# Performance work log

Hardware: AMD Instinct MI355X
Metric: run time of the kernel (lower is better)

## Reference

```python
import jax, jax.numpy as jnp
import numpy as np

N, D, K = 200000, 512, 256


def setup_inputs() -> dict:
    key = jax.random.key(0)
    ks = jax.random.split(key, 7)
    scale_in = 1.0 / np.sqrt(D)
    scale_k = 1.0 / np.sqrt(K)
    return {
        "embeds": jax.random.normal(ks[0], (N, D), dtype=jnp.float32),
        "W1": jax.random.normal(ks[1], (K, D), dtype=jnp.float32) * scale_in,
        "b1": jnp.zeros((K,), dtype=jnp.float32),
        "W2": jax.random.normal(ks[2], (K, K), dtype=jnp.float32) * scale_k,
        "b2": jnp.zeros((K,), dtype=jnp.float32),
        "W3": jax.random.normal(ks[3], (K, K), dtype=jnp.float32) * scale_k,
        "b3": jnp.zeros((K,), dtype=jnp.float32),
    }


def reference(embeds, W1, b1, W2, b2, W3, b3):
    # estimation MLP: Linear -> LeakyReLU -> Linear -> LeakyReLU -> Linear
    x = jax.nn.leaky_relu(embeds @ W1.T + b1, negative_slope=0.01)   # [N, K]
    x = jax.nn.leaky_relu(x @ W2.T + b2, negative_slope=0.01)        # [N, K]
    x = x @ W3.T + b3                                                # [N, K]
    gamma = jax.nn.softmax(x, axis=-1)                               # [N, K]
    cluster_indices = jnp.argmax(gamma, axis=-1)                     # [N]

    gamma_sum = jnp.sum(gamma, axis=0)                               # [K]
    target_gamma = jax.nn.softmax(gamma ** 2 / gamma_sum, axis=-1)   # [N, K]

    # mean: algebraically gamma^T @ embeds (avoids O(N*K*D) intermediate)
    mean = jnp.einsum('nk,nd->kd', gamma, embeds) / gamma_sum[:, None]  # [K, D]

    # F.kl_div(target_gamma.log(), gamma, reduction='sum')
    # = sum(gamma * (log gamma - log target_gamma))
    kl_loss = jnp.sum(gamma * (jnp.log(gamma) - jnp.log(target_gamma)))
    return (kl_loss, cluster_indices, mean)
```

## Files before the change

### kernel.cpp

```cpp
#include <hip/hip_runtime.h>
#include <math.h>

#define NROWS 200000
#define DIM   512
#define KC    256
#define BM    64
#define NBLK_MLP (NROWS / BM)
#define NSTEPS   (NROWS / 32)
#define MCHUNKS  125
#define MSTEPS   (NSTEPS / MCHUNKS)
#define MARGIN   0.0625f

typedef float f32x4 __attribute__((ext_vector_type(4)));
typedef short short8v __attribute__((ext_vector_type(8)));
typedef short short4v __attribute__((ext_vector_type(4)));

__device__ inline short f2bs(float f) {
  unsigned u = __float_as_uint(f);
  unsigned r = (u + 0x7FFFu + ((u >> 16) & 1u)) >> 16;
  return (short)r;
}
__device__ inline float bs2f(short s) {
  return __uint_as_float(((unsigned)(unsigned short)s) << 16);
}

__global__ __launch_bounds__(256) void transpose_kernel(const float* __restrict__ src,
                                                        float* __restrict__ dst,
                                                        int R, int C) {
  __shared__ float tile[32][33];
  const int tx = threadIdx.x;
  const int ty = threadIdx.y;
  const int c0 = blockIdx.x * 32;
  const int r0 = blockIdx.y * 32;
#pragma unroll
  for (int j = 0; j < 32; j += 8)
    tile[ty + j][tx] = src[(size_t)(r0 + ty + j) * C + c0 + tx];
  __syncthreads();
#pragma unroll
  for (int j = 0; j < 32; j += 8)
    dst[(size_t)(c0 + ty + j) * R + r0 + tx] = tile[tx][ty + j];
}

__global__ __launch_bounds__(256) void packW_kernel(const float* __restrict__ W,
                                                    short* __restrict__ P, int Kin) {
  const int KS = Kin >> 5;
  const int total = 16 * KS * 64;
  int tid = blockIdx.x * 256 + threadIdx.x;
  if (tid >= total) return;
  const int l = tid & 63;
  const int ks = (tid >> 6) % KS;
  const int nf = tid / (64 * KS);
  const float* src = W + (size_t)(nf * 16 + (l & 15)) * Kin + ks * 32 + (l >> 4) * 8;
  short8v v;
#pragma unroll
  for (int j = 0; j < 8; ++j) v[j] = f2bs(src[j]);
  *(short8v*)(P + (size_t)tid * 8) = v;
}

__global__ __launch_bounds__(256) void packE_kernel(const float* __restrict__ E,
                                                    short* __restrict__ EP) {
  const size_t s = (size_t)blockIdx.x * 256 + threadIdx.x;
  const int lane = (int)(s & 63);
  const int df = (int)((s >> 6) & 31);
  const int ns = (int)(s >> 11);
  if (ns >= NSTEPS) return;
  const int lo = lane & 15, q = lane >> 4;
  const float* src = E + ((size_t)ns * 32 + q * 8) * DIM + df * 16 + lo;
  short8v v;
#pragma unroll
  for (int j = 0; j < 8; ++j) v[j] = f2bs(src[(size_t)j * DIM]);
  *(short8v*)(EP + s * 8) = v;
}

__global__ __launch_bounds__(256, 4) void mlp_mfma_kernel(
    const float* __restrict__ E,
    const short* __restrict__ PW1, const short* __restrict__ PW2,
    const short* __restrict__ PW3,
    const float* __restrict__ b1, const float* __restrict__ b2,
    const float* __restrict__ b3,
    short* __restrict__ gammaP, float* __restrict__ idx_out,
    float* __restrict__ gsp, int* __restrict__ tiecnt, int* __restrict__ tielist) {
  __shared__ __align__(16) short X[BM * 256];
  __shared__ float redV[4][BM];
  __shared__ float redI[4][BM];
  __shared__ float red2[4][BM];
  __shared__ float rowM[BM];
  __shared__ float rowS[BM];
  __shared__ int lrows[BM];
  __shared__ int lcnt;
  __shared__ int gbase;

  const int t = threadIdx.x;
  const int blk = blockIdx.x;
  const int wc = t >> 6;
  const int lane = t & 63;
  const int lo = lane & 15;
  const int q = lane >> 4;

  if (t == 0) lcnt = 0;

  f32x4 acc[4][4];

#pragma unroll
  for (int m = 0; m < 4; ++m)
#pragma unroll
    for (int n = 0; n < 4; ++n) acc[m][n] = (f32x4){0.f, 0.f, 0.f, 0.f};

  const float* e0 = E + (size_t)(blk * BM + lo) * DIM + q * 8;
#pragma unroll
  for (int ks = 0; ks < 16; ++ks) {
    short8v a[4];
#pragma unroll
    for (int m = 0; m < 4; ++m) {
      const float* ep = e0 + m * 16 * DIM + ks * 32;
      float4 x0 = *(const float4*)ep;
      float4 x1 = *(const float4*)(ep + 4);
      short8v av;
      av[0] = f2bs(x0.x); av[1] = f2bs(x0.y); av[2] = f2bs(x0.z); av[3] = f2bs(x0.w);
      av[4] = f2bs(x1.x); av[5] = f2bs(x1.y); av[6] = f2bs(x1.z); av[7] = f2bs(x1.w);
      a[m] = av;
    }
#pragma unroll
    for (int n = 0; n < 4; ++n) {
      short8v b = *(const short8v*)(PW1 + ((size_t)((wc * 4 + n) * 16 + ks) * 64 + lane) * 8);
#pragma unroll
      for (int m = 0; m < 4; ++m)
        acc[m][n] = __builtin_amdgcn_mfma_f32_16x16x32_bf16(a[m], b, acc[m][n], 0, 0, 0);
    }
  }
  {
    float bc[4];
#pragma unroll
    for (int n = 0; n < 4; ++n) bc[n] = b1[wc * 64 + n * 16 + lo];
#pragma unroll
    for (int m = 0; m < 4; ++m)
#pragma unroll
      for (int j = 0; j < 4; ++j) {
        const int row = m * 16 + 4 * q + j;
#pragma unroll
        for (int n = 0; n < 4; ++n) {
          float v = acc[m][n][j] + bc[n];
          v = v > 0.f ? v : 0.01f * v;
          const int col = wc * 64 + n * 16 + lo;
          X[row * 256 + ((((col >> 3) ^ (row & 7)) << 3) | (col & 7))] = f2bs(v);
        }
      }
  }
  __syncthreads();

#pragma unroll
  for (int m = 0; m < 4; ++m)
#pragma unroll
    for (int n = 0; n < 4; ++n) acc[m][n] = (f32x4){0.f, 0.f, 0.f, 0.f};
#pragma unroll
  for (int ks = 0; ks < 8; ++ks) {
    short8v a[4];
#pragma unroll
    for (int m = 0; m < 4; ++m) {
      const int row = m * 16 + lo;
      const int ck = (ks * 4 + q) ^ (row & 7);
      a[m] = *(const short8v*)&X[row * 256 + ck * 8];
    }
#pragma unroll
    for (int n = 0; n < 4; ++n) {
      short8v b = *(const short8v*)(PW2 + ((size_t)((wc * 4 + n) * 8 + ks) * 64 + lane) * 8);
#pragma unroll
      for (int m = 0; m < 4; ++m)
        acc[m][n] = __builtin_amdgcn_mfma_f32_16x16x32_bf16(a[m], b, acc[m][n], 0, 0, 0);
    }
  }
  __syncthreads();
  {
    float bc[4];
#pragma unroll
    for (int n = 0; n < 4; ++n) bc[n] = b2[wc * 64 + n * 16 + lo];
#pragma unroll
    for (int m = 0; m < 4; ++m)
#pragma unroll
      for (int j = 0; j < 4; ++j) {
        const int row = m * 16 + 4 * q + j;
#pragma unroll
        for (int n = 0; n < 4; ++n) {
          float v = acc[m][n][j] + bc[n];
          v = v > 0.f ? v : 0.01f * v;
          const int col = wc * 64 + n * 16 + lo;
          X[row * 256 + ((((col >> 3) ^ (row & 7)) << 3) | (col & 7))] = f2bs(v);
        }
      }
  }
  __syncthreads();

#pragma unroll
  for (int m = 0; m < 4; ++m)
#pragma unroll
    for (int n = 0; n < 4; ++n) acc[m][n] = (f32x4){0.f, 0.f, 0.f, 0.f};
#pragma unroll
  for (int ks = 0; ks < 8; ++ks) {
    short8v a[4];
#pragma unroll
    for (int m = 0; m < 4; ++m) {
      const int row = m * 16 + lo;
      const int ck = (ks * 4 + q) ^ (row & 7);
      a[m] = *(const short8v*)&X[row * 256 + ck * 8];
    }
#pragma unroll
    for (int n = 0; n < 4; ++n) {
      short8v b = *(const short8v*)(PW3 + ((size_t)((wc * 4 + n) * 8 + ks) * 64 + lane) * 8);
#pragma unroll
      for (int m = 0; m < 4; ++m)
        acc[m][n] = __builtin_amdgcn_mfma_f32_16x16x32_bf16(a[m], b, acc[m][n], 0, 0, 0);
    }
  }
  {
    float bc[4];
#pragma unroll
    for (int n = 0; n < 4; ++n) bc[n] = b3[wc * 64 + n * 16 + lo];
#pragma unroll
    for (int m = 0; m < 4; ++m)
#pragma unroll
      for (int n = 0; n < 4; ++n)
#pragma unroll
        for (int j = 0; j < 4; ++j) acc[m][n][j] += bc[n];
  }

#pragma unroll
  for (int m = 0; m < 4; ++m)
#pragma unroll
    for (int j = 0; j < 4; ++j) {
      const int r = m * 16 + 4 * q + j;
      float mx = acc[m][0][j];
      int mi = wc * 64 + lo;
      float m2 = -3.4e38f;
#pragma unroll
      for (int n = 1; n < 4; ++n) {
        float v = acc[m][n][j];
        int c = wc * 64 + n * 16 + lo;
        if (v > mx) { m2 = mx; mx = v; mi = c; }
        else if (v > m2) m2 = v;
      }
#pragma unroll
      for (int off = 1; off < 16; off <<= 1) {
        float ov = __shfl_xor(mx, off, 64);
        int oi = __shfl_xor(mi, off, 64);
        float o2 = __shfl_xor(m2, off, 64);
        float nm2 = fmaxf(m2, o2);
        if (ov > mx) { nm2 = fmaxf(nm2, mx); mx = ov; mi = oi; }
        else { nm2 = fmaxf(nm2, ov); if (ov == mx && oi < mi) mi = oi; }
        m2 = nm2;
      }
      if (lo == 0) { redV[wc][r] = mx; redI[wc][r] = __int_as_float(mi); red2[wc][r] = m2; }
    }
  __syncthreads();

  if (t < BM) {
    float gm = -3.4e38f, g2 = -3.4e38f;
    int gi = 0;
#pragma unroll
    for (int w = 0; w < 4; ++w) {
      float v = redV[w][t];
      int i2 = __float_as_int(redI[w][t]);
      float s2 = red2[w][t];
      if (v > gm) { g2 = fmaxf(fmaxf(g2, gm), s2); gm = v; gi = i2; }
      else { if (v == gm && i2 < gi) gi = i2; g2 = fmaxf(g2, v); }
    }
    rowM[t] = gm;
    idx_out[(size_t)blk * BM + t] = (float)gi;
    if (gm - g2 < MARGIN) { int p = atomicAdd(&lcnt, 1); lrows[p] = blk * BM + t; }
  }
  __syncthreads();

#pragma unroll
  for (int m = 0; m < 4; ++m)
#pragma unroll
    for (int j = 0; j < 4; ++j) {
      const int r = m * 16 + 4 * q + j;
      const float gm = rowM[r];
      float s = 0.f;
#pragma unroll
      for (int n = 0; n < 4; ++n) {
        float e = expf(acc[m][n][j] - gm);
        acc[m][n][j] = e;
        s += e;
      }
#pragma unroll
      for (int off = 1; off < 16; off <<= 1) s += __shfl_xor(s, off, 64);
      if (lo == 0) redV[wc][r] = s;
    }
  __syncthreads();
  if (t < BM) rowS[t] = redV[0][t] + redV[1][t] + redV[2][t] + redV[3][t];
  __syncthreads();

  float csum[4] = {0.f, 0.f, 0.f, 0.f};
#pragma unroll
  for (int m = 0; m < 4; ++m)
#pragma unroll
    for (int j = 0; j < 4; ++j) {
      const int r = m * 16 + 4 * q + j;
      const float inv = 1.0f / rowS[r];
#pragma unroll
      for (int n = 0; n < 4; ++n) {
        float g = acc[m][n][j] * inv;
        csum[n] += g;
        const int col = wc * 64 + n * 16 + lo;
        X[r * 256 + ((((col >> 3) ^ (r & 7)) << 3) | (col & 7))] = f2bs(g);
      }
    }
#pragma unroll
  for (int n = 0; n < 4; ++n) {
    csum[n] += __shfl_xor(csum[n], 16, 64);
    csum[n] += __shfl_xor(csum[n], 32, 64);
  }
  if (q == 0) {
#pragma unroll
    for (int n = 0; n < 4; ++n)
      gsp[(size_t)blk * KC + wc * 64 + n * 16 + lo] = csum[n];
  }
  __syncthreads();

#pragma unroll
  for (int ns = 0; ns < 2; ++ns)
#pragma unroll
    for (int i = 0; i < 4; ++i) {
      const int kf = wc * 4 + i;
      const int k = kf * 16 + lo;
      short8v v;
#pragma unroll
      for (int j = 0; j < 8; ++j) {
        const int r = ns * 32 + q * 8 + j;
        v[j] = X[r * 256 + ((((k >> 3) ^ (r & 7)) << 3) | (k & 7))];
      }
      *(short8v*)(gammaP + ((size_t)((blk * 2 + ns) * 16 + kf) * 64 + lane) * 8) = v;
    }

  if (t == 0 && lcnt > 0) gbase = atomicAdd(tiecnt, lcnt);
  __syncthreads();
  if (t < lcnt) tielist[gbase + t] = lrows[t];
}

__global__ __launch_bounds__(256, 2) void recompute_kernel(
    const float* __restrict__ E,
    const float* __restrict__ W1T, const float* __restrict__ W2T,
    const float* __restrict__ W3T,
    const float* __restrict__ b1, const float* __restrict__ b2,
    const float* __restrict__ b3,
    const int* __restrict__ tiecnt, const int* __restrict__ tielist,
    float* __restrict__ idx_out) {
  __shared__ float Xa[32][KC];
  __shared__ float Xb[32][KC];
  __shared__ float Wt[8][KC];
  __shared__ float Et[8][32];
  __shared__ int rid[32];

  const int t = threadIdx.x;
  const int cg = t & 31;
  const int rg = t >> 5;
  const int cnt = *tiecnt;

  for (int base = blockIdx.x * 32; base < cnt; base += gridDim.x * 32) {
    const int nr = min(32, cnt - base);
    if (t < 32) rid[t] = tielist[base + min(t, nr - 1)];
    __syncthreads();

    float acc[4][2][4];
#pragma unroll
    for (int i = 0; i < 4; ++i)
#pragma unroll
      for (int j = 0; j < 2; ++j)
#pragma unroll
        for (int c = 0; c < 4; ++c) acc[i][j][c] = 0.0f;
    for (int d0 = 0; d0 < DIM; d0 += 8) {
      const float4* wsrc = (const float4*)(W1T + (size_t)d0 * KC);
      float4* wdst = (float4*)(&Wt[0][0]);
      wdst[t] = wsrc[t];
      wdst[t + 256] = wsrc[t + 256];
      Et[t & 7][t >> 3] = E[(size_t)rid[t >> 3] * DIM + d0 + (t & 7)];
      __syncthreads();
#pragma unroll
      for (int dd = 0; dd < 8; ++dd) {
        float4 e4 = *(const float4*)(&Et[dd][rg * 4]);
        float4 w0 = *(const float4*)(&Wt[dd][cg * 4]);
        float4 w1 = *(const float4*)(&Wt[dd][cg * 4 + 128]);
        float ev[4] = {e4.x, e4.y, e4.z, e4.w};
        float wv[2][4] = {{w0.x, w0.y, w0.z, w0.w}, {w1.x, w1.y, w1.z, w1.w}};
#pragma unroll
        for (int i = 0; i < 4; ++i)
#pragma unroll
          for (int j = 0; j < 2; ++j)
#pragma unroll
            for (int c = 0; c < 4; ++c)
              acc[i][j][c] = fmaf(ev[i], wv[j][c], acc[i][j][c]);
      }
      __syncthreads();
    }
    {
      float4 bb0 = *(const float4*)(b1 + cg * 4);
      float4 bb1 = *(const float4*)(b1 + cg * 4 + 128);
      float bv[2][4] = {{bb0.x, bb0.y, bb0.z, bb0.w}, {bb1.x, bb1.y, bb1.z, bb1.w}};
#pragma unroll
      for (int i = 0; i < 4; ++i)
#pragma unroll
        for (int j = 0; j < 2; ++j) {
          float4 v;
          float vv[4];
#pragma unroll
          for (int c = 0; c < 4; ++c) {
            float x = acc[i][j][c] + bv[j][c];
            vv[c] = x > 0.0f ? x : 0.01f * x;
          }
          v.x = vv[0]; v.y = vv[1]; v.z = vv[2]; v.w = vv[3];
          *(float4*)(&Xa[rg * 4 + i][cg * 4 + j * 128]) = v;
        }
    }
    __syncthreads();
#pragma unroll
    for (int i = 0; i < 4; ++i)
#pragma unroll
      for (int j = 0; j < 2; ++j)
#pragma unroll
        for (int c = 0; c < 4; ++c) acc[i][j][c] = 0.0f;
    for (int d0 = 0; d0 < KC; d0 += 8) {
      const float4* wsrc = (const float4*)(W2T + (size_t)d0 * KC);
      float4* wdst = (float4*)(&Wt[0][0]);
      wdst[t] = wsrc[t];
      wdst[t + 256] = wsrc[t + 256];
      __syncthreads();
#pragma unroll
      for (int dd = 0; dd < 8; ++dd) {
        const int d = d0 + dd;
        float ev[4];
#pragma unroll
        for (int i = 0; i < 4; ++i) ev[i] = Xa[rg * 4 + i][d];
        float4 w0 = *(const float4*)(&Wt[dd][cg * 4]);
        float4 w1 = *(const float4*)(&Wt[dd][cg * 4 + 128]);
        float wv[2][4] = {{w0.x, w0.y, w0.z, w0.w}, {w1.x, w1.y, w1.z, w1.w}};
#pragma unroll
        for (int i = 0; i < 4; ++i)
#pragma unroll
          for (int j = 0; j < 2; ++j)
#pragma unroll
            for (int c = 0; c < 4; ++c)
              acc[i][j][c] = fmaf(ev[i], wv[j][c], acc[i][j][c]);
      }
      __syncthreads();
    }
    {
      float4 bb0 = *(const float4*)(b2 + cg * 4);
      float4 bb1 = *(const float4*)(b2 + cg * 4 + 128);
      float bv[2][4] = {{bb0.x, bb0.y, bb0.z, bb0.w}, {bb1.x, bb1.y, bb1.z, bb1.w}};
#pragma unroll
      for (int i = 0; i < 4; ++i)
#pragma unroll
        for (int j = 0; j < 2; ++j) {
          float4 v;
          float vv[4];
#pragma unroll
          for (int c = 0; c < 4; ++c) {
            float x = acc[i][j][c] + bv[j][c];
            vv[c] = x > 0.0f ? x : 0.01f * x;
          }
          v.x = vv[0]; v.y = vv[1]; v.z = vv[2]; v.w = vv[3];
          *(float4*)(&Xb[rg * 4 + i][cg * 4 + j * 128]) = v;
        }
    }
    __syncthreads();
#pragma unroll
    for (int i = 0; i < 4; ++i)
#pragma unroll
      for (int j = 0; j < 2; ++j)
#pragma unroll
        for (int c = 0; c < 4; ++c) acc[i][j][c] = 0.0f;
    for (int d0 = 0; d0 < KC; d0 += 8) {
      const float4* wsrc = (const float4*)(W3T + (size_t)d0 * KC);
      float4* wdst = (float4*)(&Wt[0][0]);
      wdst[t] = wsrc[t];
      wdst[t + 256] = wsrc[t + 256];
      __syncthreads();
#pragma unroll
      for (int dd = 0; dd < 8; ++dd) {
        const int d = d0 + dd;
        float ev[4];
#pragma unroll
        for (int i = 0; i < 4; ++i) ev[i] = Xb[rg * 4 + i][d];
        float4 w0 = *(const float4*)(&Wt[dd][cg * 4]);
        float4 w1 = *(const float4*)(&Wt[dd][cg * 4 + 128]);
        float wv[2][4] = {{w0.x, w0.y, w0.z, w0.w}, {w1.x, w1.y, w1.z, w1.w}};
#pragma unroll
        for (int i = 0; i < 4; ++i)
#pragma unroll
          for (int j = 0; j < 2; ++j)
#pragma unroll
            for (int c = 0; c < 4; ++c)
              acc[i][j][c] = fmaf(ev[i], wv[j][c], acc[i][j][c]);
      }
      __syncthreads();
    }
    {
      float4 bb0 = *(const float4*)(b3 + cg * 4);
      float4 bb1 = *(const float4*)(b3 + cg * 4 + 128);
      float bv[2][4] = {{bb0.x, bb0.y, bb0.z, bb0.w}, {bb1.x, bb1.y, bb1.z, bb1.w}};
#pragma unroll
      for (int i = 0; i < 4; ++i)
#pragma unroll
        for (int j = 0; j < 2; ++j) {
          float4 v;
          v.x = acc[i][j][0] + bv[j][0];
          v.y = acc[i][j][1] + bv[j][1];
          v.z = acc[i][j][2] + bv[j][2];
          v.w = acc[i][j][3] + bv[j][3];
          *(float4*)(&Xa[rg * 4 + i][cg * 4 + j * 128]) = v;
        }
    }
    __syncthreads();
    const int wv_ = t >> 6;
    const int lane = t & 63;
#pragma unroll 1
    for (int rr = 0; rr < 8; ++rr) {
      const int lr = wv_ * 8 + rr;
      float4 x4 = *(const float4*)(&Xa[lr][lane * 4]);
      float xv[4] = {x4.x, x4.y, x4.z, x4.w};
      float bvv = xv[0];
      int bi = lane * 4;
#pragma unroll
      for (int c = 1; c < 4; ++c)
        if (xv[c] > bvv) { bvv = xv[c]; bi = lane * 4 + c; }
#pragma unroll
      for (int off = 32; off > 0; off >>= 1) {
        float ov = __shfl_xor(bvv, off, 64);
        int oi = __shfl_xor(bi, off, 64);
        if (ov > bvv || (ov == bvv && oi < bi)) { bvv = ov; bi = oi; }
      }
      if (lane == 0 && lr < nr) idx_out[rid[lr]] = (float)bi;
    }
    __syncthreads();
  }
}

__global__ __launch_bounds__(256) void gsum_reduce_kernel(const float* __restrict__ gsp,
                                                          float* __restrict__ gsum) {
  const int b = blockIdx.x;
  const int k = threadIdx.x;
  float s = 0.0f;
  for (int i = 0; i < 125; ++i) s += gsp[(size_t)(b * 125 + i) * KC + k];
  atomicAdd(&gsum[k], s);
}

__global__ __launch_bounds__(256) void kl_kernel(const short* __restrict__ gP,
                                                 const float* __restrict__ gsum,
                                                 float* __restrict__ out_kl) {
  const int t = threadIdx.x;
  const int w = t >> 6, lane = t & 63;
  const int lo = lane & 15;
  __shared__ float bsum[4];
  float kacc = 0.f;
#pragma unroll 1
  for (int it = 0; it < 2; ++it) {
    const int ns = blockIdx.x * 8 + w * 2 + it;
    if (ns < NSTEPS) {
      float s12[8], m[8], s[8];
#pragma unroll
      for (int j = 0; j < 8; ++j) { s12[j] = 0.f; m[j] = 0.f; s[j] = 0.f; }
#pragma unroll 1
      for (int kf = 0; kf < 16; ++kf) {
        short8v g8 = *(const short8v*)(gP + ((size_t)(ns * 16 + kf) * 64 + lane) * 8);
        const float rg = 1.0f / gsum[kf * 16 + lo];
#pragma unroll
        for (int j = 0; j < 8; ++j) {
          float g = bs2f(g8[j]);
          float y = g * g * rg;
          s12[j] += (g > 0.f ? g * __logf(g) : 0.f) - g * y;
          float nm = fmaxf(m[j], y);
          s[j] = s[j] * __expf(m[j] - nm) + __expf(y - nm);
          m[j] = nm;
        }
      }
#pragma unroll
      for (int off = 1; off < 16; off <<= 1) {
#pragma unroll
        for (int j = 0; j < 8; ++j) {
          float om = __shfl_xor(m[j], off, 64);
          float os = __shfl_xor(s[j], off, 64);
          float nm = fmaxf(m[j], om);
          s[j] = s[j] * __expf(m[j] - nm) + os * __expf(om - nm);
          m[j] = nm;
          s12[j] += __shfl_xor(s12[j], off, 64);
        }
      }
      if (lo == 0) {
#pragma unroll
        for (int j = 0; j < 8; ++j) kacc += s12[j] + m[j] + __logf(s[j]);
      }
    }
  }
#pragma unroll
  for (int off = 1; off < 64; off <<= 1) kacc += __shfl_xor(kacc, off, 64);
  if (lane == 0) bsum[w] = kacc;
  __syncthreads();
  if (t == 0) atomicAdd(out_kl, bsum[0] + bsum[1] + bsum[2] + bsum[3]);
}

__global__ __launch_bounds__(256, 4) void mean_mfma(const short* __restrict__ gP,
                                                    const short* __restrict__ EP,
                                                    float* __restrict__ partial) {
  const int t = threadIdx.x;
  const int w = t >> 6, lane = t & 63;
  const int kt = blockIdx.x >> 1;
  const int dt = blockIdx.x & 1;
  const int c = blockIdx.y;
  f32x4 acc[4][4];
#pragma unroll
  for (int i = 0; i < 4; ++i)
#pragma unroll
    for (int j = 0; j < 4; ++j) acc[i][j] = (f32x4){0.f, 0.f, 0.f, 0.f};

  const int ns0 = c * MSTEPS;
#pragma unroll 2
  for (int nsi = 0; nsi < MSTEPS; ++nsi) {
    const int ns = ns0 + nsi;
    short8v af[4], bf[4];
#pragma unroll
    for (int i = 0; i < 4; ++i)
      af[i] = *(const short8v*)(gP + ((size_t)(ns * 16 + kt * 4 + i) * 64 + lane) * 8);
#pragma unroll
    for (int j = 0; j < 4; ++j)
      bf[j] = *(const short8v*)(EP + ((size_t)(ns * 32 + dt * 16 + w * 4 + j) * 64 + lane) * 8);
#pragma unroll
    for (int i = 0; i < 4; ++i)
#pragma unroll
      for (int j = 0; j < 4; ++j)
        acc[i][j] = __builtin_amdgcn_mfma_f32_16x16x32_bf16(af[i], bf[j], acc[i][j], 0, 0, 0);
  }
  const int lo = lane & 15, q = lane >> 4;
  const size_t pbase = (size_t)c * (KC * DIM);
#pragma unroll
  for (int i = 0; i < 4; ++i)
#pragma unroll
    for (int j = 0; j < 4; ++j) {
      const int d = dt * 256 + w * 64 + j * 16 + lo;
#pragma unroll
      for (int r = 0; r < 4; ++r) {
        const int k = kt * 64 + i * 16 + q * 4 + r;
        partial[pbase + (size_t)k * DIM + d] = acc[i][j][r];
      }
    }
}

__global__ __launch_bounds__(256) void mean_pass2(const float* __restrict__ partial,
                                                  const float* __restrict__ gsum,
                                                  float* __restrict__ out_mean) {
  const int t = blockIdx.x * 256 + threadIdx.x;
  float s = 0.0f;
  for (int c = 0; c < MCHUNKS; ++c) s += partial[(size_t)c * (KC * DIM) + t];
  out_mean[t] = s / gsum[t >> 9];
}

extern "C" void kernel_launch(void* const* d_in, const int* in_sizes, int n_in,
                              void* d_out, int out_size, void* d_ws, size_t ws_size,
                              hipStream_t stream) {
  const float* E  = (const float*)d_in[0];
  const float* W1 = (const float*)d_in[1];
  const float* b1 = (const float*)d_in[2];
  const float* W2 = (const float*)d_in[3];
  const float* b2 = (const float*)d_in[4];
  const float* W3 = (const float*)d_in[5];
  const float* b3 = (const float*)d_in[6];
  float* out = (float*)d_out;

  char* p = (char*)d_ws;
  short* gammaP = (short*)p; p += (size_t)NROWS * KC * 2;
  short* EPb    = (short*)p; p += (size_t)NROWS * DIM * 2;
  float* gsp    = (float*)p; p += (size_t)NBLK_MLP * KC * 4;
  float* gsum   = (float*)p; p += KC * 4;
  short* pw1    = (short*)p; p += (size_t)KC * DIM * 2;
  short* pw2    = (short*)p; p += (size_t)KC * KC * 2;
  short* pw3    = (short*)p; p += (size_t)KC * KC * 2;
  float* w1t    = (float*)p; p += (size_t)DIM * KC * 4;
  float* w2t    = (float*)p; p += (size_t)KC * KC * 4;
  float* w3t    = (float*)p; p += (size_t)KC * KC * 4;
  int* tcnt     = (int*)p;   p += 256;
  int* tlist    = (int*)p;   p += (size_t)NROWS * 4;
  float* mpart  = (float*)p; p += (size_t)MCHUNKS * KC * DIM * 4;

  hipMemsetAsync(d_out, 0, sizeof(float), stream);
  hipMemsetAsync(gsum, 0, KC * sizeof(float), stream);
  hipMemsetAsync(tcnt, 0, sizeof(int), stream);

  packW_kernel<<<64, 256, 0, stream>>>(W1, pw1, DIM);
  packW_kernel<<<32, 256, 0, stream>>>(W2, pw2, KC);
  packW_kernel<<<32, 256, 0, stream>>>(W3, pw3, KC);
  transpose_kernel<<<dim3(DIM / 32, KC / 32), dim3(32, 8), 0, stream>>>(W1, w1t, KC, DIM);
  transpose_kernel<<<dim3(KC / 32, KC / 32), dim3(32, 8), 0, stream>>>(W2, w2t, KC, KC);
  transpose_kernel<<<dim3(KC / 32, KC / 32), dim3(32, 8), 0, stream>>>(W3, w3t, KC, KC);
  packE_kernel<<<50000, 256, 0, stream>>>(E, EPb);

  mlp_mfma_kernel<<<NBLK_MLP, 256, 0, stream>>>(E, pw1, pw2, pw3, b1, b2, b3,
                                                gammaP, out + 1, gsp, tcnt, tlist);
  recompute_kernel<<<960, 256, 0, stream>>>(E, w1t, w2t, w3t, b1, b2, b3,
                                            tcnt, tlist, out + 1);
  gsum_reduce_kernel<<<25, 256, 0, stream>>>(gsp, gsum);
  kl_kernel<<<(NSTEPS + 7) / 8, 256, 0, stream>>>(gammaP, gsum, out);
  mean_mfma<<<dim3(8, MCHUNKS), 256, 0, stream>>>(gammaP, EPb, mpart);
  mean_pass2<<<(KC * DIM) / 256, 256, 0, stream>>>(mpart, gsum, out + 1 + NROWS);
}
```

Baseline: 1.999 ms.

## Rewrite tie-row recompute with split-bf16 MFMA instead of scalar FP32 FMA

Rows with near-tied argmax are no longer recomputed by a scalar FP32 FMA loop. They now use bf16 MFMA with a hi/lo split (three products per tile) to approximate FP32 accuracy. Weights are packed once into hi and lo bf16 fragments, which drops the separate transpose kernels. The recompute is meant to run faster on the matrix units, at the cost of slightly lower precision than true FP32 and more register and LDS pressure.

```diff
diff --git a/kernel.cpp b/kernel.cpp
--- a/kernel.cpp
+++ b/kernel.cpp
@@ -24,25 +24,9 @@
   return __uint_as_float(((unsigned)(unsigned short)s) << 16);
 }
 
-__global__ __launch_bounds__(256) void transpose_kernel(const float* __restrict__ src,
-                                                        float* __restrict__ dst,
-                                                        int R, int C) {
-  __shared__ float tile[32][33];
-  const int tx = threadIdx.x;
-  const int ty = threadIdx.y;
-  const int c0 = blockIdx.x * 32;
-  const int r0 = blockIdx.y * 32;
-#pragma unroll
-  for (int j = 0; j < 32; j += 8)
-    tile[ty + j][tx] = src[(size_t)(r0 + ty + j) * C + c0 + tx];
-  __syncthreads();
-#pragma unroll
-  for (int j = 0; j < 32; j += 8)
-    dst[(size_t)(c0 + ty + j) * R + r0 + tx] = tile[tx][ty + j];
-}
-
 __global__ __launch_bounds__(256) void packW_kernel(const float* __restrict__ W,
-                                                    short* __restrict__ P, int Kin) {
+                                                    short* __restrict__ Ph,
+                                                    short* __restrict__ Pl, int Kin) {
   const int KS = Kin >> 5;
   const int total = 16 * KS * 64;
   int tid = blockIdx.x * 256 + threadIdx.x;
@@ -51,10 +35,16 @@
   const int ks = (tid >> 6) % KS;
   const int nf = tid / (64 * KS);
   const float* src = W + (size_t)(nf * 16 + (l & 15)) * Kin + ks * 32 + (l >> 4) * 8;
-  short8v v;
-#pragma unroll
-  for (int j = 0; j < 8; ++j) v[j] = f2bs(src[j]);
-  *(short8v*)(P + (size_t)tid * 8) = v;
+  short8v vh, vl;
+#pragma unroll
+  for (int j = 0; j < 8; ++j) {
+    float x = src[j];
+    short h = f2bs(x);
+    vh[j] = h;
+    vl[j] = f2bs(x - bs2f(h));
+  }
+  *(short8v*)(Ph + (size_t)tid * 8) = vh;
+  *(short8v*)(Pl + (size_t)tid * 8) = vl;
 }
 
 __global__ __launch_bounds__(256) void packE_kernel(const float* __restrict__ E,
@@ -337,199 +327,191 @@
   if (t < lcnt) tielist[gbase + t] = lrows[t];
 }
 
-__global__ __launch_bounds__(256, 2) void recompute_kernel(
+__global__ __launch_bounds__(256, 2) void recompute_mfma_kernel(
     const float* __restrict__ E,
-    const float* __restrict__ W1T, const float* __restrict__ W2T,
-    const float* __restrict__ W3T,
+    const short* __restrict__ PW1h, const short* __restrict__ PW1l,
+    const short* __restrict__ PW2h, const short* __restrict__ PW2l,
+    const short* __restrict__ PW3h, const short* __restrict__ PW3l,
     const float* __restrict__ b1, const float* __restrict__ b2,
     const float* __restrict__ b3,
     const int* __restrict__ tiecnt, const int* __restrict__ tielist,
     float* __restrict__ idx_out) {
-  __shared__ float Xa[32][KC];
-  __shared__ float Xb[32][KC];
-  __shared__ float Wt[8][KC];
-  __shared__ float Et[8][32];
-  __shared__ int rid[32];
+  __shared__ __align__(16) short Xh[BM * 256];
+  __shared__ __align__(16) short Xl[BM * 256];
+  __shared__ float redV[4][BM];
+  __shared__ float redI[4][BM];
+  __shared__ int rid[BM];
 
   const int t = threadIdx.x;
-  const int cg = t & 31;
-  const int rg = t >> 5;
+  const int wc = t >> 6;
+  const int lane = t & 63;
+  const int lo = lane & 15;
+  const int q = lane >> 4;
   const int cnt = *tiecnt;
 
-  for (int base = blockIdx.x * 32; base < cnt; base += gridDim.x * 32) {
-    const int nr = min(32, cnt - base);
-    if (t < 32) rid[t] = tielist[base + min(t, nr - 1)];
+  for (int base = blockIdx.x * BM; base < cnt; base += gridDim.x * BM) {
+    if (t < BM) rid[t] = tielist[min(base + t, cnt - 1)];
     __syncthreads();
 
-    float acc[4][2][4];
-#pragma unroll
-    for (int i = 0; i < 4; ++i)
-#pragma unroll
-      for (int j = 0; j < 2; ++j)
-#pragma unroll
-        for (int c = 0; c < 4; ++c) acc[i][j][c] = 0.0f;
-    for (int d0 = 0; d0 < DIM; d0 += 8) {
-      const float4* wsrc = (const float4*)(W1T + (size_t)d0 * KC);
-      float4* wdst = (float4*)(&Wt[0][0]);
-      wdst[t] = wsrc[t];
-      wdst[t + 256] = wsrc[t + 256];
-      Et[t & 7][t >> 3] = E[(size_t)rid[t >> 3] * DIM + d0 + (t & 7)];
+    int rr0[4];
+#pragma unroll
+    for (int m = 0; m < 4; ++m) rr0[m] = rid[m * 16 + lo];
+
+    f32x4 acc[4][4];
+#pragma unroll
+    for (int m = 0; m < 4; ++m)
+#pragma unroll
+      for (int n = 0; n < 4; ++n) acc[m][n] = (f32x4){0.f, 0.f, 0.f, 0.f};
+#pragma unroll 2
+    for (int ks = 0; ks < 16; ++ks) {
+      short8v ah[4], al[4];
+#pragma unroll
+      for (int m = 0; m < 4; ++m) {
+        const float* ep = E + (size_t)rr0[m] * DIM + ks * 32 + q * 8;
+        float4 x0 = *(const float4*)ep;
+        float4 x1 = *(const float4*)(ep + 4);
+        float xv[8] = {x0.x, x0.y, x0.z, x0.w, x1.x, x1.y, x1.z, x1.w};
+        short8v vh, vl;
+#pragma unroll
+        for (int j = 0; j < 8; ++j) {
+          short h = f2bs(xv[j]);
+          vh[j] = h;
+          vl[j] = f2bs(xv[j] - bs2f(h));
+        }
+        ah[m] = vh; al[m] = vl;
+      }
+#pragma unroll
+      for (int n = 0; n < 4; ++n) {
+        const size_t off = ((size_t)((wc * 4 + n) * 16 + ks) * 64 + lane) * 8;
+        short8v bh = *(const short8v*)(PW1h + off);
+        short8v bl = *(const short8v*)(PW1l + off);
+#pragma unroll
+        for (int m = 0; m < 4; ++m) {
+          acc[m][n] = __builtin_amdgcn_mfma_f32_16x16x32_bf16(ah[m], bh, acc[m][n], 0, 0, 0);
+          acc[m][n] = __builtin_amdgcn_mfma_f32_16x16x32_bf16(ah[m], bl, acc[m][n], 0, 0, 0);
+          acc[m][n] = __builtin_amdgcn_mfma_f32_16x16x32_bf16(al[m], bh, acc[m][n], 0, 0, 0);
+        }
+      }
+    }
+    {
+      float bc[4];
+#pragma unroll
+      for (int n = 0; n < 4; ++n) bc[n] = b1[wc * 64 + n * 16 + lo];
+#pragma unroll
+      for (int m = 0; m < 4; ++m)
+#pragma unroll
+        for (int j = 0; j < 4; ++j) {
+          const int row = m * 16 + 4 * q + j;
+#pragma unroll
+          for (int n = 0; n < 4; ++n) {
+            float v = acc[m][n][j] + bc[n];
+            v = v > 0.f ? v : 0.01f * v;
+            const int col = wc * 64 + n * 16 + lo;
+            const int sidx = row * 256 + ((((col >> 3) ^ (row & 7)) << 3) | (col & 7));
+            short h = f2bs(v);
+            Xh[sidx] = h;
+            Xl[sidx] = f2bs(v - bs2f(h));
+          }
+        }
+    }
+    __syncthreads();
+
+#pragma unroll 1
+    for (int layer = 0; layer < 2; ++layer) {
+      const short* Bh = layer ? PW3h : PW2h;
+      const short* Bl = layer ? PW3l : PW2l;
+      const float* bb = layer ? b3 : b2;
+#pragma unroll
+      for (int m = 0; m < 4; ++m)
+#pragma unroll
+        for (int n = 0; n < 4; ++n) acc[m][n] = (f32x4){0.f, 0.f, 0.f, 0.f};
+#pragma unroll 2
+      for (int ks = 0; ks < 8; ++ks) {
+        short8v ah[4], al[4];
+#pragma unroll
+        for (int m = 0; m < 4; ++m) {
+          const int row = m * 16 + lo;
+          const int ck = (ks * 4 + q) ^ (row & 7);
+          ah[m] = *(const short8v*)&Xh[row * 256 + ck * 8];
+          al[m] = *(const short8v*)&Xl[row * 256 + ck * 8];
+        }
+#pragma unroll
+        for (int n = 0; n < 4; ++n) {
+          const size_t off = ((size_t)((wc * 4 + n) * 8 + ks) * 64 + lane) * 8;
+          short8v bh = *(const short8v*)(Bh + off);
+          short8v bl = *(const short8v*)(Bl + off);
+#pragma unroll
+          for (int m = 0; m < 4; ++m) {
+            acc[m][n] = __builtin_amdgcn_mfma_f32_16x16x32_bf16(ah[m], bh, acc[m][n], 0, 0, 0);
+            acc[m][n] = __builtin_amdgcn_mfma_f32_16x16x32_bf16(ah[m], bl, acc[m][n], 0, 0, 0);
+            acc[m][n] = __builtin_amdgcn_mfma_f32_16x16x32_bf16(al[m], bh, acc[m][n], 0, 0, 0);
+          }
+        }
+      }
       __syncthreads();
-#pragma unroll
-      for (int dd = 0; dd < 8; ++dd) {
-        float4 e4 = *(const float4*)(&Et[dd][rg * 4]);
-        float4 w0 = *(const float4*)(&Wt[dd][cg * 4]);
-        float4 w1 = *(const float4*)(&Wt[dd][cg * 4 + 128]);
-        float ev[4] = {e4.x, e4.y, e4.z, e4.w};
-        float wv[2][4] = {{w0.x, w0.y, w0.z, w0.w}, {w1.x, w1.y, w1.z, w1.w}};
-#pragma unroll
-        for (int i = 0; i < 4; ++i)
-#pragma unroll
-          for (int j = 0; j < 2; ++j)
-#pragma unroll
-            for (int c = 0; c < 4; ++c)
-              acc[i][j][c] = fmaf(ev[i], wv[j][c], acc[i][j][c]);
-      }
-      __syncthreads();
-    }
-    {
-      float4 bb0 = *(const float4*)(b1 + cg * 4);
-      float4 bb1 = *(const float4*)(b1 + cg * 4 + 128);
-      float bv[2][4] = {{bb0.x, bb0.y, bb0.z, bb0.w}, {bb1.x, bb1.y, bb1.z, bb1.w}};
-#pragma unroll
-      for (int i = 0; i < 4; ++i)
-#pragma unroll
-        for (int j = 0; j < 2; ++j) {
-          float4 v;
-          float vv[4];
-#pragma unroll
-          for (int c = 0; c < 4; ++c) {
-            float x = acc[i][j][c] + bv[j][c];
-            vv[c] = x > 0.0f ? x : 0.01f * x;
+      float bc[4];
+#pragma unroll
+      for (int n = 0; n < 4; ++n) bc[n] = bb[wc * 64 + n * 16 + lo];
+      if (layer == 0) {
+#pragma unroll
+        for (int m = 0; m < 4; ++m)
+#pragma unroll
+          for (int j = 0; j < 4; ++j) {
+            const int row = m * 16 + 4 * q + j;
+#pragma unroll
+            for (int n = 0; n < 4; ++n) {
+              float v = acc[m][n][j] + bc[n];
+              v = v > 0.f ? v : 0.01f * v;
+              const int col = wc * 64 + n * 16 + lo;
+              const int sidx = row * 256 + ((((col >> 3) ^ (row & 7)) << 3) | (col & 7));
+              short h = f2bs(v);
+              Xh[sidx] = h;
+              Xl[sidx] = f2bs(v - bs2f(h));
+            }
           }
-          v.x = vv[0]; v.y = vv[1]; v.z = vv[2]; v.w = vv[3];
-          *(float4*)(&Xa[rg * 4 + i][cg * 4 + j * 128]) = v;
-        }
-    }
+        __syncthreads();
+      } else {
+#pragma unroll
+        for (int m = 0; m < 4; ++m)
+#pragma unroll
+          for (int n = 0; n < 4; ++n)
+#pragma unroll
+            for (int j = 0; j < 4; ++j) acc[m][n][j] += bc[n];
+      }
+    }
+
+#pragma unroll
+    for (int m = 0; m < 4; ++m)
+#pragma unroll
+      for (int j = 0; j < 4; ++j) {
+        const int r = m * 16 + 4 * q + j;
+        float mx = acc[m][0][j];
+        int mi = wc * 64 + lo;
+#pragma unroll
+        for (int n = 1; n < 4; ++n) {
+          float v = acc[m][n][j];
+          int c = wc * 64 + n * 16 + lo;
+          if (v > mx || (v == mx && c < mi)) { mx = v; mi = c; }
+        }
+#pragma unroll
+        for (int off = 1; off < 16; off <<= 1) {
+          float ov = __shfl_xor(mx, off, 64);
+          int oi = __shfl_xor(mi, off, 64);
+          if (ov > mx || (ov == mx && oi < mi)) { mx = ov; mi = oi; }
+        }
+        if (lo == 0) { redV[wc][r] = mx; redI[wc][r] = __int_as_float(mi); }
+      }
     __syncthreads();
-#pragma unroll
-    for (int i = 0; i < 4; ++i)
-#pragma unroll
-      for (int j = 0; j < 2; ++j)
-#pragma unroll
-        for (int c = 0; c < 4; ++c) acc[i][j][c] = 0.0f;
-    for (int d0 = 0; d0 < KC; d0 += 8) {
-      const float4* wsrc = (const float4*)(W2T + (size_t)d0 * KC);
-      float4* wdst = (float4*)(&Wt[0][0]);
-      wdst[t] = wsrc[t];
-      wdst[t + 256] = wsrc[t + 256];
-      __syncthreads();
-#pragma unroll
-      for (int dd = 0; dd < 8; ++dd) {
-        const int d = d0 + dd;
-        float ev[4];
-#pragma unroll
-        for (int i = 0; i < 4; ++i) ev[i] = Xa[rg * 4 + i][d];
-        float4 w0 = *(const float4*)(&Wt[dd][cg * 4]);
-        float4 w1 = *(const float4*)(&Wt[dd][cg * 4 + 128]);
-        float wv[2][4] = {{w0.x, w0.y, w0.z, w0.w}, {w1.x, w1.y, w1.z, w1.w}};
-#pragma unroll
-        for (int i = 0; i < 4; ++i)
-#pragma unroll
-          for (int j = 0; j < 2; ++j)
-#pragma unroll
-            for (int c = 0; c < 4; ++c)
-              acc[i][j][c] = fmaf(ev[i], wv[j][c], acc[i][j][c]);
-      }
-      __syncthreads();
-    }
-    {
-      float4 bb0 = *(const float4*)(b2 + cg * 4);
-      float4 bb1 = *(const float4*)(b2 + cg * 4 + 128);
-      float bv[2][4] = {{bb0.x, bb0.y, bb0.z, bb0.w}, {bb1.x, bb1.y, bb1.z, bb1.w}};
-#pragma unroll
-      for (int i = 0; i < 4; ++i)
-#pragma unroll
-        for (int j = 0; j < 2; ++j) {
-          float4 v;
-          float vv[4];
-#pragma unroll
-          for (int c = 0; c < 4; ++c) {
-            float x = acc[i][j][c] + bv[j][c];
-            vv[c] = x > 0.0f ? x : 0.01f * x;
-          }
-          v.x = vv[0]; v.y = vv[1]; v.z = vv[2]; v.w = vv[3];
-          *(float4*)(&Xb[rg * 4 + i][cg * 4 + j * 128]) = v;
-        }
-    }
-    __syncthreads();
-#pragma unroll
-    for (int i = 0; i < 4; ++i)
-#pragma unroll
-      for (int j = 0; j < 2; ++j)
-#pragma unroll
-        for (int c = 0; c < 4; ++c) acc[i][j][c] = 0.0f;
-    for (int d0 = 0; d0 < KC; d0 += 8) {
-      const float4* wsrc = (const float4*)(W3T + (size_t)d0 * KC);
-      float4* wdst = (float4*)(&Wt[0][0]);
-      wdst[t] = wsrc[t];
-      wdst[t + 256] = wsrc[t + 256];
-      __syncthreads();
-#pragma unroll
-      for (int dd = 0; dd < 8; ++dd) {
-        const int d = d0 + dd;
-        float ev[4];
-#pragma unroll
-        for (int i = 0; i < 4; ++i) ev[i] = Xb[rg * 4 + i][d];
-        float4 w0 = *(const float4*)(&Wt[dd][cg * 4]);
-        float4 w1 = *(const float4*)(&Wt[dd][cg * 4 + 128]);
-        float wv[2][4] = {{w0.x, w0.y, w0.z, w0.w}, {w1.x, w1.y, w1.z, w1.w}};
-#pragma unroll
-        for (int i = 0; i < 4; ++i)
-#pragma unroll
-          for (int j = 0; j < 2; ++j)
-#pragma unroll
-            for (int c = 0; c < 4; ++c)
-              acc[i][j][c] = fmaf(ev[i], wv[j][c], acc[i][j][c]);
-      }
-      __syncthreads();
-    }
-    {
-      float4 bb0 = *(const float4*)(b3 + cg * 4);
-      float4 bb1 = *(const float4*)(b3 + cg * 4 + 128);
-      float bv[2][4] = {{bb0.x, bb0.y, bb0.z, bb0.w}, {bb1.x, bb1.y, bb1.z, bb1.w}};
-#pragma unroll
-      for (int i = 0; i < 4; ++i)
-#pragma unroll
-        for (int j = 0; j < 2; ++j) {
-          float4 v;
-          v.x = acc[i][j][0] + bv[j][0];
-          v.y = acc[i][j][1] + bv[j][1];
-          v.z = acc[i][j][2] + bv[j][2];
-          v.w = acc[i][j][3] + bv[j][3];
-          *(float4*)(&Xa[rg * 4 + i][cg * 4 + j * 128]) = v;
-        }
-    }
-    __syncthreads();
-    const int wv_ = t >> 6;
-    const int lane = t & 63;
-#pragma unroll 1
-    for (int rr = 0; rr < 8; ++rr) {
-      const int lr = wv_ * 8 + rr;
-      float4 x4 = *(const float4*)(&Xa[lr][lane * 4]);
-      float xv[4] = {x4.x, x4.y, x4.z, x4.w};
-      float bvv = xv[0];
-      int bi = lane * 4;
-#pragma unroll
-      for (int c = 1; c < 4; ++c)
-        if (xv[c] > bvv) { bvv = xv[c]; bi = lane * 4 + c; }
-#pragma unroll
-      for (int off = 32; off > 0; off >>= 1) {
-        float ov = __shfl_xor(bvv, off, 64);
-        int oi = __shfl_xor(bi, off, 64);
-        if (ov > bvv || (ov == bvv && oi < bi)) { bvv = ov; bi = oi; }
-      }
-      if (lane == 0 && lr < nr) idx_out[rid[lr]] = (float)bi;
+    if (t < BM) {
+      float gm = -3.4e38f;
+      int gi = 0;
+#pragma unroll
+      for (int w = 0; w < 4; ++w) {
+        float v = redV[w][t];
+        int i2 = __float_as_int(redI[w][t]);
+        if (v > gm || (v == gm && i2 < gi)) { gm = v; gi = i2; }
+      }
+      idx_out[rid[t]] = (float)gi;
     }
     __syncthreads();
   }
@@ -670,12 +652,12 @@
   short* EPb    = (short*)p; p += (size_t)NROWS * DIM * 2;
   float* gsp    = (float*)p; p += (size_t)NBLK_MLP * KC * 4;
   float* gsum   = (float*)p; p += KC * 4;
-  short* pw1    = (short*)p; p += (size_t)KC * DIM * 2;
-  short* pw2    = (short*)p; p += (size_t)KC * KC * 2;
-  short* pw3    = (short*)p; p += (size_t)KC * KC * 2;
-  float* w1t    = (float*)p; p += (size_t)DIM * KC * 4;
-  float* w2t    = (float*)p; p += (size_t)KC * KC * 4;
-  float* w3t    = (float*)p; p += (size_t)KC * KC * 4;
+  short* pw1h   = (short*)p; p += (size_t)KC * DIM * 2;
+  short* pw1l   = (short*)p; p += (size_t)KC * DIM * 2;
+  short* pw2h   = (short*)p; p += (size_t)KC * KC * 2;
+  short* pw2l   = (short*)p; p += (size_t)KC * KC * 2;
+  short* pw3h   = (short*)p; p += (size_t)KC * KC * 2;
+  short* pw3l   = (short*)p; p += (size_t)KC * KC * 2;
   int* tcnt     = (int*)p;   p += 256;
   int* tlist    = (int*)p;   p += (size_t)NROWS * 4;
   float* mpart  = (float*)p; p += (size_t)MCHUNKS * KC * DIM * 4;
@@ -684,18 +666,15 @@
   hipMemsetAsync(gsum, 0, KC * sizeof(float), stream);
   hipMemsetAsync(tcnt, 0, sizeof(int), stream);
 
-  packW_kernel<<<64, 256, 0, stream>>>(W1, pw1, DIM);
-  packW_kernel<<<32, 256, 0, stream>>>(W2, pw2, KC);
-  packW_kernel<<<32, 256, 0, stream>>>(W3, pw3, KC);
-  transpose_kernel<<<dim3(DIM / 32, KC / 32), dim3(32, 8), 0, stream>>>(W1, w1t, KC, DIM);
-  transpose_kernel<<<dim3(KC / 32, KC / 32), dim3(32, 8), 0, stream>>>(W2, w2t, KC, KC);
-  transpose_kernel<<<dim3(KC / 32, KC / 32), dim3(32, 8), 0, stream>>>(W3, w3t, KC, KC);
+  packW_kernel<<<64, 256, 0, stream>>>(W1, pw1h, pw1l, DIM);
+  packW_kernel<<<32, 256, 0, stream>>>(W2, pw2h, pw2l, KC);
+  packW_kernel<<<32, 256, 0, stream>>>(W3, pw3h, pw3l, KC);
   packE_kernel<<<50000, 256, 0, stream>>>(E, EPb);
 
-  mlp_mfma_kernel<<<NBLK_MLP, 256, 0, stream>>>(E, pw1, pw2, pw3, b1, b2, b3,
+  mlp_mfma_kernel<<<NBLK_MLP, 256, 0, stream>>>(E, pw1h, pw2h, pw3h, b1, b2, b3,
                                                 gammaP, out + 1, gsp, tcnt, tlist);
-  recompute_kernel<<<960, 256, 0, stream>>>(E, w1t, w2t, w3t, b1, b2, b3,
-                                            tcnt, tlist, out + 1);
+  recompute_mfma_kernel<<<512, 256, 0, stream>>>(E, pw1h, pw1l, pw2h, pw2l, pw3h, pw3l,
+                                                 b1, b2, b3, tcnt, tlist, out + 1);
   gsum_reduce_kernel<<<25, 256, 0, stream>>>(gsp, gsum);
   kl_kernel<<<(NSTEPS + 7) / 8, 256, 0, stream>>>(gammaP, gsum, out);
   mean_mfma<<<dim3(8, MCHUNKS), 256, 0, stream>>>(gammaP, EPb, mpart);
```

Measured after the change: 1.605 ms. 19.7% less time.
